# Performance work log

Hardware: AMD Instinct MI355X
Metric: run time of the kernel (lower is better)

## Reference

```python
import jax, jax.numpy as jnp
import numpy as np

SIZE = 512
K = 100000.0
EPS = 1e-05


def setup_inputs() -> dict:
    key = jax.random.key(0)
    contour = jax.random.uniform(key, (128, 2), dtype=jnp.float32)
    return {"contour": contour}


def reference(contour):
    size, k, eps = SIZE, K, EPS
    # mesh: (size^2, 1, 2), normalized pixel coordinates (ij indexing like torch.meshgrid)
    coords = jnp.arange(size, dtype=jnp.float32)
    mesh = jnp.stack(jnp.meshgrid(coords, coords, indexing="ij"), axis=-1)
    mesh = mesh.reshape(-1, 1, 2) / size

    diff = contour[None, :, :] - mesh              # (P, N, 2), P = size^2
    roll_diff = jnp.roll(diff, -1, axis=1)          # next contour point
    # roll by 1 along a size-2 axis == swap (x, y)
    prod = diff * roll_diff[:, :, ::-1]             # (P, N, 2)
    sign = jnp.tanh(k * (prod[:, :, 1] - prod[:, :, 0]))  # cross-product sign

    norm_diff = jnp.linalg.norm(diff, axis=2)
    norm_roll = jnp.linalg.norm(roll_diff, axis=2)
    scalar_product = jnp.sum(diff * roll_diff, axis=2)
    cos_ang = jnp.clip(scalar_product / (norm_diff * norm_roll), -1.0 + eps, 1.0 - eps)
    angles = jnp.arccos(cos_ang)                    # (P, N)

    sum_angles = jnp.clip(jnp.sum(sign * angles, axis=1) / (2.0 * jnp.pi), 0.0, 1.0)
    return sum_angles.reshape(1, 1, size, size)
```

## Files before the change

kernel.cpp:

```cpp
#include <hip/hip_runtime.h>
#include <math.h>

#define SIZE 512
#define NPTS 128

__global__ __launch_bounds__(256) void contour_mask_kernel(
    const float* __restrict__ contour, float* __restrict__ out)
{
    __shared__ float2 c[NPTS + 1];

    const int tid = threadIdx.x;
    if (tid < NPTS)  c[tid]  = ((const float2*)contour)[tid];
    if (tid == NPTS) c[NPTS] = ((const float2*)contour)[0];
    __syncthreads();

    const int p = blockIdx.x * 256 + tid;
    const int i = p >> 9;
    const int j = p & (SIZE - 1);

    const float mx = (float)i * (1.0f / SIZE);
    const float my = (float)j * (1.0f / SIZE);

    const float K    = 100000.0f;
    const float PI_F = 3.14159265358979f;
    const float HPI  = 1.57079632679490f;
    const float INV2PI = 0.15915494309190f;
    const float ANG_LO = 4.4721397e-3f;
    const float ANG_HI = 3.1371205f;
    const float CTHR = 6e-5f;

    float ax = c[0].x - mx;
    float ay = c[0].y - my;

    float w    = 0.0f;
    float corr = 0.0f;

    #pragma unroll 1
    for (int g = 0; g < NPTS / 8; ++g) {
        const float gax = ax, gay = ay;
        float bmin = 1e30f;

        #pragma unroll
        for (int k = 0; k < 8; ++k) {
            const float2 cn = c[g * 8 + k + 1];
            const float bx = cn.x - mx;
            const float by = cn.y - my;
            const float cr = fmaf(ay, bx, -ax * by);
            const bool inc = (ay >  0.0f) & (by <= 0.0f) & (cr > 0.0f);
            const bool dec = (ay <= 0.0f) & (by >  0.0f) & (cr < 0.0f);
            w += inc ? 1.0f : 0.0f;
            w -= dec ? 1.0f : 0.0f;
            bmin = fminf(bmin, fabsf(cr));
            ax = bx; ay = by;
        }

        if (__any(bmin < CTHR)) {
            float fax = gax, fay = gay;
            #pragma unroll
            for (int k = 0; k < 8; ++k) {
                const float2 cn = c[g * 8 + k + 1];
                const float bx = cn.x - mx;
                const float by = cn.y - my;
                const float cr = fmaf(fay, bx, -fax * by);
                const float dt = fmaf(fax, bx,  fay * by);

                const float acr = fabsf(cr), adt = fabsf(dt);
                const float mn  = fminf(acr, adt);
                const float mxv = fmaxf(acr, adt);
                const float t   = mn * __builtin_amdgcn_rcpf(mxv);
                const float s2  = t * t;
                float q = fmaf(-0.01172120f, s2, 0.05265332f);
                q = fmaf(q, s2, -0.11643287f);
                q = fmaf(q, s2,  0.19354346f);
                q = fmaf(q, s2, -0.33262347f);
                q = fmaf(q, s2,  0.99997726f);
                float an = t * q;
                an = (acr > adt) ? (HPI  - an) : an;
                an = (dt < 0.0f) ? (PI_F - an) : an;
                const float anc = __builtin_amdgcn_fmed3f(an, ANG_LO, ANG_HI);

                const float e  = __expf(2.0f * K * cr);
                const float th = fmaf(-2.0f, __builtin_amdgcn_rcpf(e + 1.0f), 1.0f);

                corr += fmaf(th, anc, -__builtin_copysignf(an, cr));

                fax = bx; fay = by;
            }
        }
    }

    const float r = fmaf(corr, INV2PI, w);
    out[p] = __builtin_amdgcn_fmed3f(r, 0.0f, 1.0f);
}

extern "C" void kernel_launch(void* const* d_in, const int* in_sizes, int n_in,
                              void* d_out, int out_size, void* d_ws, size_t ws_size,
                              hipStream_t stream) {
    const float* contour = (const float*)d_in[0];
    float* out = (float*)d_out;

    const int total = SIZE * SIZE;
    const int block = 256;
    const int grid  = total / block;

    contour_mask_kernel<<<grid, block, 0, stream>>>(contour, out);
}
```

Baseline: 73.49 us.

## Check the near-edge correction per edge and simplify winding-number arithmetic

Replaces the two-pass scheme, which scanned groups of 8 edges and then recomputed all 8 when any lane came near an edge, with a single loop that tests each edge with a wavefront vote and computes the angle/tanh correction only for that edge. The winding-number update is rewritten with an up/down indicator difference, which cuts the comparisons per edge. This avoids recomputing crossing terms and doing 8 corrections where one would do, at the cost of a vote and branch on every edge instead of every 8.

```diff
diff --git a/kernel.cpp b/kernel.cpp
--- a/kernel.cpp
+++ b/kernel.cpp
@@ -31,62 +31,47 @@
 
     float ax = c[0].x - mx;
     float ay = c[0].y - my;
+    float uy = (ay > 0.0f) ? 1.0f : 0.0f;
 
     float w    = 0.0f;
     float corr = 0.0f;
 
-    #pragma unroll 1
-    for (int g = 0; g < NPTS / 8; ++g) {
-        const float gax = ax, gay = ay;
-        float bmin = 1e30f;
+    #pragma unroll 8
+    for (int n = 0; n < NPTS; ++n) {
+        const float2 cn = c[n + 1];
+        const float bx = cn.x - mx;
+        const float by = cn.y - my;
+        const float cr = fmaf(ay, bx, -ax * by);
 
-        #pragma unroll
-        for (int k = 0; k < 8; ++k) {
-            const float2 cn = c[g * 8 + k + 1];
-            const float bx = cn.x - mx;
-            const float by = cn.y - my;
-            const float cr = fmaf(ay, bx, -ax * by);
-            const bool inc = (ay >  0.0f) & (by <= 0.0f) & (cr > 0.0f);
-            const bool dec = (ay <= 0.0f) & (by >  0.0f) & (cr < 0.0f);
-            w += inc ? 1.0f : 0.0f;
-            w -= dec ? 1.0f : 0.0f;
-            bmin = fminf(bmin, fabsf(cr));
-            ax = bx; ay = by;
+        const float vy = (by > 0.0f) ? 1.0f : 0.0f;
+        const float d  = uy - vy;
+        const float m  = d * cr;
+        w += (m > 0.0f) ? d : 0.0f;
+
+        if (__any(fabsf(cr) < CTHR)) {
+            const float dt  = fmaf(ax, bx, ay * by);
+            const float acr = fabsf(cr), adt = fabsf(dt);
+            const float mn  = fminf(acr, adt);
+            const float mxv = fmaxf(acr, adt);
+            const float t   = mn * __builtin_amdgcn_rcpf(mxv);
+            const float s2  = t * t;
+            float q = fmaf(-0.01172120f, s2, 0.05265332f);
+            q = fmaf(q, s2, -0.11643287f);
+            q = fmaf(q, s2,  0.19354346f);
+            q = fmaf(q, s2, -0.33262347f);
+            q = fmaf(q, s2,  0.99997726f);
+            float an = t * q;
+            an = (acr > adt) ? (HPI  - an) : an;
+            an = (dt < 0.0f) ? (PI_F - an) : an;
+            const float anc = __builtin_amdgcn_fmed3f(an, ANG_LO, ANG_HI);
+
+            const float e  = __expf(2.0f * K * cr);
+            const float th = fmaf(-2.0f, __builtin_amdgcn_rcpf(e + 1.0f), 1.0f);
+
+            corr += fmaf(th, anc, -__builtin_copysignf(an, cr));
         }
 
-        if (__any(bmin < CTHR)) {
-            float fax = gax, fay = gay;
-            #pragma unroll
-            for (int k = 0; k < 8; ++k) {
-                const float2 cn = c[g * 8 + k + 1];
-                const float bx = cn.x - mx;
-                const float by = cn.y - my;
-                const float cr = fmaf(fay, bx, -fax * by);
-                const float dt = fmaf(fax, bx,  fay * by);
-
-                const float acr = fabsf(cr), adt = fabsf(dt);
-                const float mn  = fminf(acr, adt);
-                const float mxv = fmaxf(acr, adt);
-                const float t   = mn * __builtin_amdgcn_rcpf(mxv);
-                const float s2  = t * t;
-                float q = fmaf(-0.01172120f, s2, 0.05265332f);
-                q = fmaf(q, s2, -0.11643287f);
-                q = fmaf(q, s2,  0.19354346f);
-                q = fmaf(q, s2, -0.33262347f);
-                q = fmaf(q, s2,  0.99997726f);
-                float an = t * q;
-                an = (acr > adt) ? (HPI  - an) : an;
-                an = (dt < 0.0f) ? (PI_F - an) : an;
-                const float anc = __builtin_amdgcn_fmed3f(an, ANG_LO, ANG_HI);
-
-                const float e  = __expf(2.0f * K * cr);
-                const float th = fmaf(-2.0f, __builtin_amdgcn_rcpf(e + 1.0f), 1.0f);
-
-                corr += fmaf(th, anc, -__builtin_copysignf(an, cr));
-
-                fax = bx; fay = by;
-            }
-        }
+        ax = bx; ay = by; uy = vy;
     }
 
     const float r = fmaf(corr, INV2PI, w);
```

After: 64.44 us (median of 2 runs). -12.3%, faster.
